# Kernel optimization log

Hardware: AMD Instinct MI355X
Metric: run time of the kernel (lower is better)

## Reference

```python
import jax, jax.numpy as jnp
import numpy as np

N = 50000
IN_CH = 128
HID = 32
HEADS = 3
OUT_CH = 128
E = 800000
NEG_SLOPE = 0.2
BN_EPS = 1e-5


def _glorot(key, shape):
    fan = shape[0] + shape[-1]
    s = jnp.sqrt(6.0 / fan)
    return jax.random.uniform(key, shape, jnp.float32, -s, s)


def setup_inputs() -> dict:
    key = jax.random.key(0)
    ks = jax.random.split(key, 12)
    x = jax.random.normal(ks[0], (N, IN_CH), jnp.float32)
    edge_index = jax.random.randint(ks[1], (2, E), 0, N, jnp.int64)
    # GATConv 1: in -> HID per head, HEADS heads, concat
    W1 = _glorot(ks[2], (IN_CH, HEADS * HID))
    att_src1 = _glorot(ks[3], (HEADS, HID))
    att_dst1 = _glorot(ks[4], (HEADS, HID))
    b1 = jnp.zeros((HEADS * HID,), jnp.float32)
    # GATConv 2: HEADS*HID -> OUT_CH, 1 head
    W2 = _glorot(ks[5], (HEADS * HID, OUT_CH))
    att_src2 = _glorot(ks[6], (1, OUT_CH))
    att_dst2 = _glorot(ks[7], (1, OUT_CH))
    b2 = jnp.zeros((OUT_CH,), jnp.float32)
    # BatchNorm params
    bn_gamma = jnp.ones((OUT_CH,), jnp.float32)
    bn_beta = jnp.zeros((OUT_CH,), jnp.float32)
    # residual Linear
    Wres = _glorot(ks[8], (IN_CH, OUT_CH))
    bres = jnp.zeros((OUT_CH,), jnp.float32)
    return dict(x=x, edge_index=edge_index, W1=W1, att_src1=att_src1,
                att_dst1=att_dst1, b1=b1, W2=W2, att_src2=att_src2,
                att_dst2=att_dst2, b2=b2, bn_gamma=bn_gamma, bn_beta=bn_beta,
                Wres=Wres, bres=bres)


def gat_conv(x, W, a_src, a_dst, b, src, dst, n, heads, ch):
    """PyG GATConv (eval mode, self-loops already in src/dst)."""
    h = (x @ W).reshape(n, heads, ch)                    # [N,H,C]
    a_s = jnp.sum(h * a_src[None], axis=-1)              # [N,H]
    a_d = jnp.sum(h * a_dst[None], axis=-1)              # [N,H]
    e = a_s[src] + a_d[dst]                              # [E,H]
    e = jnp.where(e > 0, e, NEG_SLOPE * e)               # leaky_relu
    m = jax.ops.segment_max(e, dst, num_segments=n)      # softmax over edges into dst
    e = jnp.exp(e - m[dst])
    denom = jax.ops.segment_sum(e, dst, num_segments=n)
    alpha = e / (denom[dst] + 1e-16)                     # [E,H]
    out = jax.ops.segment_sum(h[src] * alpha[:, :, None], dst, num_segments=n)
    return out.reshape(n, heads * ch) + b


def reference(x, edge_index, W1, att_src1, att_dst1, b1, W2, att_src2,
              att_dst2, b2, bn_gamma, bn_beta, Wres, bres):
    n = x.shape[0]
    loop = jnp.arange(n, dtype=edge_index.dtype)
    src = jnp.concatenate([edge_index[0], loop])         # add self-loops (PyG default)
    dst = jnp.concatenate([edge_index[1], loop])
    residual = x @ Wres + bres
    out = gat_conv(x, W1, att_src1, att_dst1, b1, src, dst, n, HEADS, HID)
    out = gat_conv(out, W2, att_src2, att_dst2, b2, src, dst, n, 1, OUT_CH)
    # BatchNorm1d, training-mode batch statistics
    mu = jnp.mean(out, axis=0)
    var = jnp.var(out, axis=0)
    out = (out - mu) * jax.lax.rsqrt(var + BN_EPS) * bn_gamma + bn_beta
    out = jax.nn.relu(out)
    return out + residual
```

## Files before the change

kernel.cpp:

```cpp
#include <hip/hip_runtime.h>

#define NEG 0.2f
#define NEG_INF (-1e30f)

typedef __attribute__((ext_vector_type(8))) short bf16x8;
typedef __attribute__((ext_vector_type(4))) float f32x4;

__device__ __forceinline__ float leaky(float e) { return e > 0.f ? e : NEG * e; }

__device__ __forceinline__ unsigned short f2bf(float f) {
    unsigned int u = __float_as_uint(f);
    unsigned int r = u + 0x7fffu + ((u >> 16) & 1u);
    return (unsigned short)(r >> 16);
}
__device__ __forceinline__ float2 bf2f2(unsigned int u) {
    float2 r;
    r.x = __uint_as_float(u << 16);
    r.y = __uint_as_float(u & 0xffff0000u);
    return r;
}

__device__ __forceinline__ void pack_w(const float* __restrict__ W,
                                       unsigned short* __restrict__ Bp, int K, int N, int idx) {
    int i = idx & 7;
    int rest = idx >> 3;
    int lane = rest & 63;
    rest >>= 6;
    int KT = K / 32;
    int kt = rest % KT;
    int ct = rest / KT;
    int m = lane & 15, kb = lane >> 4;
    int k = kt * 32 + kb * 8 + i, col = ct * 16 + m;
    Bp[idx] = f2bf(W[(size_t)k * N + col]);
}

__global__ __launch_bounds__(256) void prep_kernel(const float* __restrict__ x,
                                                   unsigned short* __restrict__ xb, int n4,
                                                   const float* __restrict__ W1,
                                                   unsigned short* __restrict__ w1p,
                                                   const float* __restrict__ W2,
                                                   unsigned short* __restrict__ w2p,
                                                   const float* __restrict__ Wres,
                                                   unsigned short* __restrict__ wresp,
                                                   const int* __restrict__ dst, int E,
                                                   int* __restrict__ bucketCnt, int nbk,
                                                   int binBlks) {
    int b = blockIdx.x;
    if (b < binBlks) {
        __shared__ int hist[1600];
        for (int k = threadIdx.x; k < nbk; k += 256) hist[k] = 0;
        __syncthreads();
        int c0 = b * 4096;
        int cnt = min(4096, E - c0);
        for (int i = threadIdx.x; i < cnt; i += 256)
            atomicAdd(&hist[dst[c0 + i] >> 5], 1);
        __syncthreads();
        for (int k = threadIdx.x; k < nbk; k += 256) {
            int h = hist[k];
            if (h) atomicAdd(&bucketCnt[k], h);
        }
        return;
    }
    b -= binBlks;
    int nxb = (n4 + 255) / 256;
    if (b < nxb) {
        int i = b * 256 + threadIdx.x;
        if (i < n4) {
            float4 v = ((const float4*)x)[i];
            ushort4 o;
            o.x = f2bf(v.x); o.y = f2bf(v.y); o.z = f2bf(v.z); o.w = f2bf(v.w);
            ((ushort4*)xb)[i] = o;
        }
        return;
    }
    b -= nxb;
    if (b < 48) { pack_w(W1, w1p, 128, 96, b * 256 + threadIdx.x); return; }
    b -= 48;
    if (b < 48) { pack_w(W2, w2p, 96, 128, b * 256 + threadIdx.x); return; }
    b -= 48;
    if (b < 64) { pack_w(Wres, wresp, 128, 128, b * 256 + threadIdx.x); }
}

__global__ __launch_bounds__(1024) void scan_buckets(const int* __restrict__ bc,
                                                     int* __restrict__ pairBase,
                                                     int* __restrict__ bcur,
                                                     int* __restrict__ offs, int nbk, int n,
                                                     float* __restrict__ part) {
    __shared__ int buf[1024];
    __shared__ int carry;
    int tid = threadIdx.x;
    for (int i = tid; i < 64 * 256; i += 1024) part[i] = 0.f;
    if (tid == 0) carry = 0;
    __syncthreads();
    for (int base = 0; base < nbk; base += 1024) {
        int v = (base + tid < nbk) ? bc[base + tid] : 0;
        buf[tid] = v;
        __syncthreads();
        for (int s = 1; s < 1024; s <<= 1) {
            int t = (tid >= s) ? buf[tid - s] : 0;
            __syncthreads();
            buf[tid] += t;
            __syncthreads();
        }
        int incl = buf[tid];
        int tot = buf[1023];
        int c = carry;
        if (base + tid < nbk) {
            int ex = c + incl - v;
            pairBase[base + tid] = ex;
            bcur[base + tid] = ex;
        }
        __syncthreads();
        if (tid == 0) carry = c + tot;
        __syncthreads();
    }
    if (tid == 0) {
        pairBase[nbk] = carry;
        offs[n] = carry;
    }
}

__global__ __launch_bounds__(256) void bin_kernel(const int* __restrict__ src,
                                                  const int* __restrict__ dst, int E,
                                                  int* __restrict__ bcur,
                                                  int2* __restrict__ pairBuf, int nb) {
    __shared__ int2 stage[4096];
    __shared__ int hist[1600];
    __shared__ int base[1600];
    for (int c0 = blockIdx.x * 4096; c0 < E; c0 += gridDim.x * 4096) {
        int cnt = min(4096, E - c0);
        for (int b = threadIdx.x; b < nb; b += 256) hist[b] = 0;
        __syncthreads();
        for (int i = threadIdx.x; i < cnt; i += 256) {
            int s = src[c0 + i], d = dst[c0 + i];
            stage[i] = make_int2(s, d);
            atomicAdd(&hist[d >> 5], 1);
        }
        __syncthreads();
        for (int b = threadIdx.x; b < nb; b += 256) {
            int h = hist[b];
            if (h) base[b] = atomicAdd(&bcur[b], h);
            hist[b] = 0;
        }
        __syncthreads();
        for (int i = threadIdx.x; i < cnt; i += 256) {
            int2 p = stage[i];
            int b = p.y >> 5;
            int off = atomicAdd(&hist[b], 1);
            pairBuf[base[b] + off] = p;
        }
        __syncthreads();
    }
}

template <int K, int N, int HEADS>
__device__ __forceinline__ void gemm_body(int w, const unsigned short* __restrict__ A,
                                          const unsigned short* __restrict__ Bp,
                                          const float* __restrict__ bias,
                                          unsigned short* __restrict__ outB,
                                          const float* __restrict__ asrc,
                                          const float* __restrict__ adst,
                                          float* __restrict__ a_s,
                                          float* __restrict__ a_d, int M) {
    constexpr int KT = K / 32, CT = N / 16;
    int row0 = w * 16;
    if (row0 >= M) return;
    int lane = threadIdx.x & 63;
    int m = lane & 15, kb = lane >> 4;
    const unsigned short* arow = A + (size_t)(row0 + m) * K + kb * 8;

    f32x4 acc[CT];
#pragma unroll
    for (int ct = 0; ct < CT; ++ct) acc[ct] = (f32x4){0.f, 0.f, 0.f, 0.f};

#pragma unroll
    for (int kt = 0; kt < KT; ++kt) {
        bf16x8 a = *(const bf16x8*)(arow + kt * 32);
#pragma unroll
        for (int ct = 0; ct < CT; ++ct) {
            bf16x8 b = *(const bf16x8*)(Bp + ((size_t)(ct * KT + kt) * 64 + lane) * 8);
            acc[ct] = __builtin_amdgcn_mfma_f32_16x16x32_bf16(a, b, acc[ct], 0, 0, 0);
        }
    }

#pragma unroll
    for (int r = 0; r < 4; ++r) {
        int row = row0 + kb * 4 + r;
#pragma unroll
        for (int ct = 0; ct < CT; ++ct) {
            int col = ct * 16 + m;
            float v = acc[ct][r] + (bias ? bias[col] : 0.f);
            outB[(size_t)row * N + col] = f2bf(v);
        }
    }

    if (HEADS > 0) {
        float asv[CT], adv[CT];
#pragma unroll
        for (int ct = 0; ct < CT; ++ct) {
            int col = ct * 16 + m;
            asv[ct] = asrc[col];
            adv[ct] = adst[col];
        }
        constexpr int TPH = CT / (HEADS > 0 ? HEADS : 1);
#pragma unroll
        for (int r = 0; r < 4; ++r) {
            int row = row0 + kb * 4 + r;
#pragma unroll
            for (int h = 0; h < HEADS; ++h) {
                float s = 0.f, d = 0.f;
#pragma unroll
                for (int t = 0; t < TPH; ++t) {
                    int ct = h * TPH + t;
                    s += acc[ct][r] * asv[ct];
                    d += acc[ct][r] * adv[ct];
                }
#pragma unroll
                for (int off = 1; off <= 8; off <<= 1) {
                    s += __shfl_xor(s, off);
                    d += __shfl_xor(d, off);
                }
                if (m == 0) {
                    a_s[(size_t)row * HEADS + h] = s;
                    a_d[(size_t)row * HEADS + h] = d;
                }
            }
        }
    }
}

__global__ __launch_bounds__(256) void phase2_kernel(
    const int2* __restrict__ pairBuf, const int* __restrict__ pairBase,
    const int* __restrict__ bcur, int* __restrict__ offs,
    int* __restrict__ csr, int nb,
    const unsigned short* __restrict__ xb,
    const unsigned short* __restrict__ w1p, unsigned short* __restrict__ h1b,
    const float* __restrict__ asrc1, const float* __restrict__ adst1,
    float* __restrict__ as1, float* __restrict__ ad1,
    const unsigned short* __restrict__ wresp, const float* __restrict__ bres,
    unsigned short* __restrict__ residb, int n, int passBlks, int g1Blks) {
    int b = blockIdx.x;
    int lane = threadIdx.x & 63;
    int wid = threadIdx.x >> 6;
    if (b < passBlks) {
        __shared__ int cnt[4][32];
        int bk = b * 4 + wid;
        if (bk < nb) {
            int node0 = bk * 32;
            int lo = pairBase[bk], hi = bcur[bk];
            if (lane < 32) cnt[wid][lane] = 0;
            for (int i = lo + lane; i < hi; i += 64)
                atomicAdd(&cnt[wid][pairBuf[i].y & 31], 1);
            int myc = (lane < 32) ? cnt[wid][lane] : 0;
            int c = myc;
#pragma unroll
            for (int s = 1; s < 32; s <<= 1) {
                int t = __shfl_up(c, s);
                if (lane >= s && lane < 32) c += t;
            }
            int basePos = lo + c - myc;
            if (lane < 32) {
                if (node0 + lane < n) offs[node0 + lane] = basePos;
                cnt[wid][lane] = basePos;
            }
            for (int i = lo + lane; i < hi; i += 64) {
                int2 p = pairBuf[i];
                int pos = atomicAdd(&cnt[wid][p.y & 31], 1);
                csr[pos] = p.x;
            }
        }
        return;
    }
    b -= passBlks;
    if (b < g1Blks) {
        gemm_body<128, 96, 3>(b * 4 + wid, xb, w1p, nullptr, h1b,
                              asrc1, adst1, as1, ad1, n);
        return;
    }
    b -= g1Blks;
    gemm_body<128, 128, 0>(b * 4 + wid, xb, wresp, bres, residb,
                           nullptr, nullptr, nullptr, nullptr, n);
}

__global__ __launch_bounds__(256) void gemm2_kernel(const unsigned short* __restrict__ A,
                                                    const unsigned short* __restrict__ Bp,
                                                    unsigned short* __restrict__ outB,
                                                    const float* __restrict__ asrc,
                                                    const float* __restrict__ adst,
                                                    float* __restrict__ a_s,
                                                    float* __restrict__ a_d, int M) {
    gemm_body<96, 128, 1>(blockIdx.x * 4 + (threadIdx.x >> 6), A, Bp, nullptr, outB,
                          asrc, adst, a_s, a_d, M);
}

__global__ __launch_bounds__(256) void gat1_agg(const unsigned short* __restrict__ h1b,
                                                const float* __restrict__ a_s,
                                                const float* __restrict__ a_d,
                                                const int* __restrict__ offs,
                                                const int* __restrict__ csr,
                                                const float* __restrict__ b1,
                                                unsigned short* __restrict__ out1b, int n) {
    __shared__ int ssrc[4][64];
    __shared__ float se[4][3][64];
    int wid = threadIdx.x >> 6;
    int node = blockIdx.x * 4 + wid;
    if (node >= n) return;
    int lane = threadIdx.x & 63;
    int head = lane >> 4; if (head > 2) head = 2;
    int beg = offs[node], end = offs[node + 1];
    int deg = end - beg;
    float ad0 = a_d[node * 3 + 0], ad1 = a_d[node * 3 + 1], ad2 = a_d[node * 3 + 2];
    float es0 = leaky(a_s[node * 3 + 0] + ad0);
    float es1 = leaky(a_s[node * 3 + 1] + ad1);
    float es2 = leaky(a_s[node * 3 + 2] + ad2);
    float2 hv0 = make_float2(0.f, 0.f);
    if (lane < 48) hv0 = bf2f2(*(const unsigned int*)&h1b[(size_t)node * 96 + 2 * lane]);

    float den;
    float2 acc;

    if (deg <= 64) {
        int s = 0;
        float l0 = NEG_INF, l1 = NEG_INF, l2 = NEG_INF;
        if (lane < deg) {
            s = csr[beg + lane];
            l0 = leaky(a_s[s * 3 + 0] + ad0);
            l1 = leaky(a_s[s * 3 + 1] + ad1);
            l2 = leaky(a_s[s * 3 + 2] + ad2);
        }
        float m0 = l0, m1 = l1, m2 = l2;
#pragma unroll
        for (int sh = 32; sh >= 1; sh >>= 1) {
            m0 = fmaxf(m0, __shfl_xor(m0, sh));
            m1 = fmaxf(m1, __shfl_xor(m1, sh));
            m2 = fmaxf(m2, __shfl_xor(m2, sh));
        }
        m0 = fmaxf(m0, es0); m1 = fmaxf(m1, es1); m2 = fmaxf(m2, es2);
        float e0 = 0.f, e1 = 0.f, e2 = 0.f;
        if (lane < deg) {
            e0 = __expf(l0 - m0); e1 = __expf(l1 - m1); e2 = __expf(l2 - m2);
        }
        ssrc[wid][lane] = s;
        se[wid][0][lane] = e0; se[wid][1][lane] = e1; se[wid][2][lane] = e2;
        float w0 = __expf(es0 - m0), w1 = __expf(es1 - m1), w2 = __expf(es2 - m2);
        den = (head == 0) ? w0 : ((head == 1) ? w1 : w2);
        float wSelf = (lane < 16) ? w0 : ((lane < 32) ? w1 : w2);
        acc.x = wSelf * hv0.x; acc.y = wSelf * hv0.y;

        int jj = 0;
        for (; jj + 7 < deg; jj += 8) {
            int sA[8]; float wA[8]; unsigned ph[8];
#pragma unroll
            for (int q = 0; q < 8; ++q) {
                sA[q] = ssrc[wid][jj + q];
                wA[q] = se[wid][head][jj + q];
            }
#pragma unroll
            for (int q = 0; q < 8; ++q)
                ph[q] = (lane < 48) ? *(const unsigned*)&h1b[(size_t)sA[q] * 96 + 2 * lane] : 0u;
            float dsum = 0.f;
#pragma unroll
            for (int q = 0; q < 8; ++q) {
                dsum += wA[q];
                if (lane < 48) {
                    float2 h = bf2f2(ph[q]);
                    acc.x += wA[q] * h.x; acc.y += wA[q] * h.y;
                }
            }
            den += dsum;
        }
        for (; jj + 3 < deg; jj += 4) {
            int sA[4]; float wA[4]; unsigned ph[4];
#pragma unroll
            for (int q = 0; q < 4; ++q) {
                sA[q] = ssrc[wid][jj + q];
                wA[q] = se[wid][head][jj + q];
            }
#pragma unroll
            for (int q = 0; q < 4; ++q)
                ph[q] = (lane < 48) ? *(const unsigned*)&h1b[(size_t)sA[q] * 96 + 2 * lane] : 0u;
            float dsum = 0.f;
#pragma unroll
            for (int q = 0; q < 4; ++q) {
                dsum += wA[q];
                if (lane < 48) {
                    float2 h = bf2f2(ph[q]);
                    acc.x += wA[q] * h.x; acc.y += wA[q] * h.y;
                }
            }
            den += dsum;
        }
        for (; jj < deg; ++jj) {
            int sA = ssrc[wid][jj];
            float wA = se[wid][head][jj];
            den += wA;
            if (lane < 48) {
                float2 ha = bf2f2(*(const unsigned*)&h1b[(size_t)sA * 96 + 2 * lane]);
                acc.x += wA * ha.x; acc.y += wA * ha.y;
            }
        }
    } else {
        float m0 = es0, m1 = es1, m2 = es2;
        for (int j = beg + lane; j < end; j += 64) {
            int s = csr[j];
            m0 = fmaxf(m0, leaky(a_s[s * 3 + 0] + ad0));
            m1 = fmaxf(m1, leaky(a_s[s * 3 + 1] + ad1));
            m2 = fmaxf(m2, leaky(a_s[s * 3 + 2] + ad2));
        }
#pragma unroll
        for (int sh = 32; sh >= 1; sh >>= 1) {
            m0 = fmaxf(m0, __shfl_xor(m0, sh));
            m1 = fmaxf(m1, __shfl_xor(m1, sh));
            m2 = fmaxf(m2, __shfl_xor(m2, sh));
        }
        float w0 = __expf(es0 - m0), w1 = __expf(es1 - m1), w2 = __expf(es2 - m2);
        den = (head == 0) ? w0 : ((head == 1) ? w1 : w2);
        float wSelf = (lane < 16) ? w0 : ((lane < 32) ? w1 : w2);
        acc.x = wSelf * hv0.x; acc.y = wSelf * hv0.y;
        for (int t0 = beg; t0 < end; t0 += 64) {
            int cnt = min(64, end - t0);
            int s = 0;
            float e0 = 0.f, e1 = 0.f, e2 = 0.f;
            if (lane < cnt) {
                s = csr[t0 + lane];
                e0 = __expf(leaky(a_s[s * 3 + 0] + ad0) - m0);
                e1 = __expf(leaky(a_s[s * 3 + 1] + ad1) - m1);
                e2 = __expf(leaky(a_s[s * 3 + 2] + ad2) - m2);
            }
            ssrc[wid][lane] = s;
            se[wid][0][lane] = e0; se[wid][1][lane] = e1; se[wid][2][lane] = e2;
            int jj = 0;
            for (; jj + 7 < cnt; jj += 8) {
                int sA[8]; float wA[8]; unsigned ph[8];
#pragma unroll
                for (int q = 0; q < 8; ++q) {
                    sA[q] = ssrc[wid][jj + q];
                    wA[q] = se[wid][head][jj + q];
                }
#pragma unroll
                for (int q = 0; q < 8; ++q)
                    ph[q] = (lane < 48) ? *(const unsigned*)&h1b[(size_t)sA[q] * 96 + 2 * lane] : 0u;
                float dsum = 0.f;
#pragma unroll
                for (int q = 0; q < 8; ++q) {
                    dsum += wA[q];
                    if (lane < 48) {
                        float2 h = bf2f2(ph[q]);
                        acc.x += wA[q] * h.x; acc.y += wA[q] * h.y;
                    }
                }
                den += dsum;
            }
            for (; jj < cnt; ++jj) {
                int sA = ssrc[wid][jj];
                float wA = se[wid][head][jj];
                den += wA;
                if (lane < 48) {
                    float2 ha = bf2f2(*(const unsigned*)&h1b[(size_t)sA * 96 + 2 * lane]);
                    acc.x += wA * ha.x; acc.y += wA * ha.y;
                }
            }
        }
    }

    if (lane < 48) {
        float inv = 1.f / (den + 1e-16f);
        ushort2 o;
        o.x = f2bf(acc.x * inv + b1[2 * lane]);
        o.y = f2bf(acc.y * inv + b1[2 * lane + 1]);
        *(ushort2*)&out1b[(size_t)node * 96 + 2 * lane] = o;
    }
}

__global__ __launch_bounds__(256) void gat2_agg(const unsigned short* __restrict__ h2b,
                                                const float* __restrict__ a_s,
                                                const float* __restrict__ a_d,
                                                const int* __restrict__ offs,
                                                const int* __restrict__ csr,
                                                const float* __restrict__ b2,
                                                unsigned short* __restrict__ out2b,
                                                float* __restrict__ part, int n) {
    __shared__ int ssrc[4][64];
    __shared__ float se[4][64];
    __shared__ float4 red[4][64];
    int wid = threadIdx.x >> 6;
    int node = blockIdx.x * 4 + wid;
    int lane = threadIdx.x & 63;
    float2 o = make_float2(0.f, 0.f);

    if (node < n) {
        int beg = offs[node], end = offs[node + 1];
        int deg = end - beg;
        float ad = a_d[node];
        float es = leaky(a_s[node] + ad);
        float2 hv0 = bf2f2(*(const unsigned int*)&h2b[(size_t)node * 128 + 2 * lane]);
        float den;
        float2 acc;

        if (deg <= 64) {
            int s = 0;
            float l = NEG_INF;
            if (lane < deg) {
                s = csr[beg + lane];
                l = leaky(a_s[s] + ad);
            }
            float m = l;
#pragma unroll
            for (int sh = 32; sh >= 1; sh >>= 1) m = fmaxf(m, __shfl_xor(m, sh));
            m = fmaxf(m, es);
            float e = (lane < deg) ? __expf(l - m) : 0.f;
            ssrc[wid][lane] = s;
            se[wid][lane] = e;
            float wSelf = __expf(es - m);
            den = wSelf;
            acc.x = wSelf * hv0.x; acc.y = wSelf * hv0.y;

            int jj = 0;
            for (; jj + 7 < deg; jj += 8) {
                int sA[8]; float wA[8]; unsigned ph[8];
#pragma unroll
                for (int q = 0; q < 8; ++q) {
                    sA[q] = ssrc[wid][jj + q];
                    wA[q] = se[wid][jj + q];
                }
#pragma unroll
                for (int q = 0; q < 8; ++q)
                    ph[q] = *(const unsigned*)&h2b[(size_t)sA[q] * 128 + 2 * lane];
                float dsum = 0.f;
#pragma unroll
                for (int q = 0; q < 8; ++q) {
                    dsum += wA[q];
                    float2 h = bf2f2(ph[q]);
                    acc.x += wA[q] * h.x; acc.y += wA[q] * h.y;
                }
                den += dsum;
            }
            for (; jj + 3 < deg; jj += 4) {
                int sA[4]; float wA[4]; unsigned ph[4];
#pragma unroll
                for (int q = 0; q < 4; ++q) {
                    sA[q] = ssrc[wid][jj + q];
                    wA[q] = se[wid][jj + q];
                }
#pragma unroll
                for (int q = 0; q < 4; ++q)
                    ph[q] = *(const unsigned*)&h2b[(size_t)sA[q] * 128 + 2 * lane];
                float dsum = 0.f;
#pragma unroll
                for (int q = 0; q < 4; ++q) {
                    dsum += wA[q];
                    float2 h = bf2f2(ph[q]);
                    acc.x += wA[q] * h.x; acc.y += wA[q] * h.y;
                }
                den += dsum;
            }
            for (; jj < deg; ++jj) {
                int sA = ssrc[wid][jj];
                float wA = se[wid][jj];
                den += wA;
                float2 ha = bf2f2(*(const unsigned*)&h2b[(size_t)sA * 128 + 2 * lane]);
                acc.x += wA * ha.x; acc.y += wA * ha.y;
            }
        } else {
            float m = es;
            for (int j = beg + lane; j < end; j += 64) {
                int s = csr[j];
                m = fmaxf(m, leaky(a_s[s] + ad));
            }
#pragma unroll
            for (int sh = 32; sh >= 1; sh >>= 1) m = fmaxf(m, __shfl_xor(m, sh));
            float wSelf = __expf(es - m);
            den = wSelf;
            acc.x = wSelf * hv0.x; acc.y = wSelf * hv0.y;
            for (int t0 = beg; t0 < end; t0 += 64) {
                int cnt = min(64, end - t0);
                int s = 0;
                float e = 0.f;
                if (lane < cnt) {
                    s = csr[t0 + lane];
                    e = __expf(leaky(a_s[s] + ad) - m);
                }
                ssrc[wid][lane] = s;
                se[wid][lane] = e;
                int jj = 0;
                for (; jj + 7 < cnt; jj += 8) {
                    int sA[8]; float wA[8]; unsigned ph[8];
#pragma unroll
                    for (int q = 0; q < 8; ++q) {
                        sA[q] = ssrc[wid][jj + q];
                        wA[q] = se[wid][jj + q];
                    }
#pragma unroll
                    for (int q = 0; q < 8; ++q)
                        ph[q] = *(const unsigned*)&h2b[(size_t)sA[q] * 128 + 2 * lane];
                    float dsum = 0.f;
#pragma unroll
                    for (int q = 0; q < 8; ++q) {
                        dsum += wA[q];
                        float2 h = bf2f2(ph[q]);
                        acc.x += wA[q] * h.x; acc.y += wA[q] * h.y;
                    }
                    den += dsum;
                }
                for (; jj < cnt; ++jj) {
                    int sA = ssrc[wid][jj];
                    float wA = se[wid][jj];
                    den += wA;
                    float2 ha = bf2f2(*(const unsigned*)&h2b[(size_t)sA * 128 + 2 * lane]);
                    acc.x += wA * ha.x; acc.y += wA * ha.y;
                }
            }
        }

        float inv = 1.f / (den + 1e-16f);
        o.x = acc.x * inv + b2[2 * lane];
        o.y = acc.y * inv + b2[2 * lane + 1];
        ushort2 ob;
        ob.x = f2bf(o.x); ob.y = f2bf(o.y);
        *(ushort2*)&out2b[(size_t)node * 128 + 2 * lane] = ob;
    }

    red[wid][lane] = make_float4(o.x, o.y, o.x * o.x, o.y * o.y);
    __syncthreads();
    if (wid == 0) {
        float4 a = red[0][lane], b = red[1][lane], c = red[2][lane], d = red[3][lane];
        float sx = a.x + b.x + c.x + d.x;
        float sy = a.y + b.y + c.y + d.y;
        float qx = a.z + b.z + c.z + d.z;
        float qy = a.w + b.w + c.w + d.w;
        float* p = part + (size_t)(blockIdx.x & 63) * 256;
        atomicAdd(&p[2 * lane + 0], sx);
        atomicAdd(&p[2 * lane + 1], sy);
        atomicAdd(&p[128 + 2 * lane + 0], qx);
        atomicAdd(&p[128 + 2 * lane + 1], qy);
    }
}

__global__ void bn_finalize(const float* __restrict__ part, const float* __restrict__ gamma,
                            const float* __restrict__ beta, float* __restrict__ ss, int n) {
    int c = threadIdx.x;
    float S = 0.f, Q = 0.f;
    for (int k = 0; k < 64; ++k) {
        S += part[(size_t)k * 256 + c];
        Q += part[(size_t)k * 256 + 128 + c];
    }
    float invN = 1.f / (float)n;
    float mu = S * invN;
    float var = Q * invN - mu * mu;
    float g = gamma[c] * rsqrtf(var + 1e-5f);
    ss[c] = g;
    ss[128 + c] = beta[c] - mu * g;
}

__global__ void final_kernel(const unsigned short* __restrict__ out2b,
                             const unsigned short* __restrict__ residb,
                             const float* __restrict__ ss, float* __restrict__ out, int n) {
    int i = blockIdx.x * blockDim.x + threadIdx.x;
    if (i >= n * 32) return;
    int c0 = (i & 31) * 4;
    uint2 v = ((const uint2*)out2b)[i];
    uint2 r = ((const uint2*)residb)[i];
    float2 v01 = bf2f2(v.x), v23 = bf2f2(v.y);
    float2 r01 = bf2f2(r.x), r23 = bf2f2(r.y);
    float4 o;
    o.x = fmaxf(v01.x * ss[c0 + 0] + ss[128 + c0 + 0], 0.f) + r01.x;
    o.y = fmaxf(v01.y * ss[c0 + 1] + ss[128 + c0 + 1], 0.f) + r01.y;
    o.z = fmaxf(v23.x * ss[c0 + 2] + ss[128 + c0 + 2], 0.f) + r23.x;
    o.w = fmaxf(v23.y * ss[c0 + 3] + ss[128 + c0 + 3], 0.f) + r23.y;
    ((float4*)out)[i] = o;
}

extern "C" void kernel_launch(void* const* d_in, const int* in_sizes, int n_in,
                              void* d_out, int out_size, void* d_ws, size_t ws_size,
                              hipStream_t stream) {
    const float* x     = (const float*)d_in[0];
    const int*   ei    = (const int*)d_in[1];
    const float* W1    = (const float*)d_in[2];
    const float* asrc1 = (const float*)d_in[3];
    const float* adst1 = (const float*)d_in[4];
    const float* b1    = (const float*)d_in[5];
    const float* W2    = (const float*)d_in[6];
    const float* asrc2 = (const float*)d_in[7];
    const float* adst2 = (const float*)d_in[8];
    const float* b2    = (const float*)d_in[9];
    const float* gamma = (const float*)d_in[10];
    const float* beta  = (const float*)d_in[11];
    const float* Wres  = (const float*)d_in[12];
    const float* bres  = (const float*)d_in[13];

    const int n = in_sizes[0] / 128;
    const int E = in_sizes[1] / 2;

    char* ws = (char*)d_ws;
    size_t off = 0;
    auto alloc = [&](size_t bytes) {
        void* p = ws + off;
        off = (off + bytes + 255) & ~(size_t)255;
        return p;
    };
    float* as1  = (float*)alloc((size_t)n * 3 * 4);
    float* ad1  = (float*)alloc((size_t)n * 3 * 4);
    float* as2  = (float*)alloc((size_t)n * 4);
    float* ad2  = (float*)alloc((size_t)n * 4);
    float* part = (float*)alloc(64 * 256 * 4);
    float* ss   = (float*)alloc(256 * 4);
    unsigned short* xb     = (unsigned short*)alloc((size_t)n * 128 * 2);
    unsigned short* h1b    = (unsigned short*)alloc((size_t)n * 96 * 2);
    unsigned short* h2b    = (unsigned short*)alloc((size_t)n * 128 * 2);
    unsigned short* out1b  = (unsigned short*)alloc((size_t)n * 96 * 2);
    unsigned short* out2b  = (unsigned short*)alloc((size_t)n * 128 * 2);
    unsigned short* residb = (unsigned short*)alloc((size_t)n * 128 * 2);
    unsigned short* w1p    = (unsigned short*)alloc(128 * 96 * 2);
    unsigned short* w2p    = (unsigned short*)alloc(96 * 128 * 2);
    unsigned short* wresp  = (unsigned short*)alloc(128 * 128 * 2);
    int* offs      = (int*)alloc((size_t)(n + 1) * 4);
    int* bucketCnt = (int*)alloc(1600 * 4);
    int* pairBase  = (int*)alloc(1601 * 4);
    int* bcur      = (int*)alloc(1600 * 4);
    int2* pairBuf  = (int2*)alloc((size_t)E * 8);
    int* csr       = (int*)alloc((size_t)E * 4);

    hipMemsetAsync(bucketCnt, 0, 1600 * 4, stream);

    const int* srcIdx = ei;
    const int* dstIdx = ei + E;
    const int NB = (n + 31) / 32;
    const int binBlks = (E + 4095) / 4096;

    const int nxb = (n * 32 + 255) / 256;
    prep_kernel<<<binBlks + nxb + 160, 256, 0, stream>>>(x, xb, n * 32, W1, w1p, W2, w2p,
                                                         Wres, wresp, dstIdx, E,
                                                         bucketCnt, NB, binBlks);

    scan_buckets<<<1, 1024, 0, stream>>>(bucketCnt, pairBase, bcur, offs, NB, n, part);

    bin_kernel<<<binBlks, 256, 0, stream>>>(srcIdx, dstIdx, E, bcur, pairBuf, NB);

    const int mt = (n + 15) / 16;
    const int gblk = (mt + 3) / 4;
    const int passBlks = 391;

    phase2_kernel<<<passBlks + 2 * gblk, 256, 0, stream>>>(
        pairBuf, pairBase, bcur, offs, csr, NB, xb, w1p, h1b, asrc1, adst1, as1, ad1,
        wresp, bres, residb, n, passBlks, gblk);

    gat1_agg<<<(n + 3) / 4, 256, 0, stream>>>(h1b, as1, ad1, offs, csr, b1, out1b, n);
    gemm2_kernel<<<gblk, 256, 0, stream>>>(out1b, w2p, h2b, asrc2, adst2, as2, ad2, n);
    gat2_agg<<<(n + 3) / 4, 256, 0, stream>>>(h2b, as2, ad2, offs, csr, b2, out2b, part, n);
    bn_finalize<<<1, 128, 0, stream>>>(part, gamma, beta, ss, n);
    final_kernel<<<(n * 32 + 255) / 256, 256, 0, stream>>>(out2b, residb, ss, (float*)d_out, n);
}
```

Measured before the change: 163.9 us.

## Split wavefront into two halves processing alternate edges with 8-byte gathers

Both GAT aggregation kernels now split each 64-lane wave into two halves that process alternate neighbor edges, with each lane gathering 4 bf16 features (8 bytes) instead of 2. The two halves' partial sums are combined with a cross-half shuffle at the end. The softmax denominator is now computed with a wave reduction over the exp values instead of being accumulated serially in the gather loop. This is meant to double the number of edge gathers in flight and widen the loads, in exchange for extra shuffles and reworked BN partial-sum bookkeeping.

```diff
diff --git a/kernel.cpp b/kernel.cpp
--- a/kernel.cpp
+++ b/kernel.cpp
@@ -306,18 +306,21 @@
     int node = blockIdx.x * 4 + wid;
     if (node >= n) return;
     int lane = threadIdx.x & 63;
-    int head = lane >> 4; if (head > 2) head = 2;
+    int half = lane >> 5;
+    int cl = lane & 31;
+    int c4 = cl * 4;
+    bool act = cl < 24;
+    int head4 = act ? (cl >> 3) : 2;
+
     int beg = offs[node], end = offs[node + 1];
     int deg = end - beg;
     float ad0 = a_d[node * 3 + 0], ad1 = a_d[node * 3 + 1], ad2 = a_d[node * 3 + 2];
     float es0 = leaky(a_s[node * 3 + 0] + ad0);
     float es1 = leaky(a_s[node * 3 + 1] + ad1);
     float es2 = leaky(a_s[node * 3 + 2] + ad2);
-    float2 hv0 = make_float2(0.f, 0.f);
-    if (lane < 48) hv0 = bf2f2(*(const unsigned int*)&h1b[(size_t)node * 96 + 2 * lane]);
-
-    float den;
-    float2 acc;
+
+    float den0, den1, den2;
+    float a0 = 0.f, a1 = 0.f, a2 = 0.f, a3 = 0.f;
 
     if (deg <= 64) {
         int s = 0;
@@ -342,61 +345,53 @@
         }
         ssrc[wid][lane] = s;
         se[wid][0][lane] = e0; se[wid][1][lane] = e1; se[wid][2][lane] = e2;
+        float d0 = e0, d1 = e1, d2 = e2;
+#pragma unroll
+        for (int sh = 32; sh >= 1; sh >>= 1) {
+            d0 += __shfl_xor(d0, sh);
+            d1 += __shfl_xor(d1, sh);
+            d2 += __shfl_xor(d2, sh);
+        }
         float w0 = __expf(es0 - m0), w1 = __expf(es1 - m1), w2 = __expf(es2 - m2);
-        den = (head == 0) ? w0 : ((head == 1) ? w1 : w2);
-        float wSelf = (lane < 16) ? w0 : ((lane < 32) ? w1 : w2);
-        acc.x = wSelf * hv0.x; acc.y = wSelf * hv0.y;
-
+        den0 = d0 + w0; den1 = d1 + w1; den2 = d2 + w2;
+        if (half == 0 && act) {
+            uint2 hv = *(const uint2*)&h1b[(size_t)node * 96 + c4];
+            float wS = (head4 == 0) ? w0 : ((head4 == 1) ? w1 : w2);
+            float2 x01 = bf2f2(hv.x), x23 = bf2f2(hv.y);
+            a0 = wS * x01.x; a1 = wS * x01.y; a2 = wS * x23.x; a3 = wS * x23.y;
+        }
         int jj = 0;
         for (; jj + 7 < deg; jj += 8) {
-            int sA[8]; float wA[8]; unsigned ph[8];
-#pragma unroll
-            for (int q = 0; q < 8; ++q) {
-                sA[q] = ssrc[wid][jj + q];
-                wA[q] = se[wid][head][jj + q];
-            }
-#pragma unroll
-            for (int q = 0; q < 8; ++q)
-                ph[q] = (lane < 48) ? *(const unsigned*)&h1b[(size_t)sA[q] * 96 + 2 * lane] : 0u;
-            float dsum = 0.f;
-#pragma unroll
-            for (int q = 0; q < 8; ++q) {
-                dsum += wA[q];
-                if (lane < 48) {
-                    float2 h = bf2f2(ph[q]);
-                    acc.x += wA[q] * h.x; acc.y += wA[q] * h.y;
-                }
-            }
-            den += dsum;
-        }
-        for (; jj + 3 < deg; jj += 4) {
-            int sA[4]; float wA[4]; unsigned ph[4];
-#pragma unroll
-            for (int q = 0; q < 4; ++q) {
-                sA[q] = ssrc[wid][jj + q];
-                wA[q] = se[wid][head][jj + q];
-            }
-#pragma unroll
-            for (int q = 0; q < 4; ++q)
-                ph[q] = (lane < 48) ? *(const unsigned*)&h1b[(size_t)sA[q] * 96 + 2 * lane] : 0u;
-            float dsum = 0.f;
-#pragma unroll
-            for (int q = 0; q < 4; ++q) {
-                dsum += wA[q];
-                if (lane < 48) {
-                    float2 h = bf2f2(ph[q]);
-                    acc.x += wA[q] * h.x; acc.y += wA[q] * h.y;
-                }
-            }
-            den += dsum;
-        }
-        for (; jj < deg; ++jj) {
-            int sA = ssrc[wid][jj];
-            float wA = se[wid][head][jj];
-            den += wA;
-            if (lane < 48) {
-                float2 ha = bf2f2(*(const unsigned*)&h1b[(size_t)sA * 96 + 2 * lane]);
-                acc.x += wA * ha.x; acc.y += wA * ha.y;
+            int eA = jj + half, eB = jj + 2 + half, eC = jj + 4 + half, eD = jj + 6 + half;
+            int sA = ssrc[wid][eA], sB = ssrc[wid][eB];
+            int sC = ssrc[wid][eC], sD = ssrc[wid][eD];
+            float wA = se[wid][head4][eA], wB = se[wid][head4][eB];
+            float wC = se[wid][head4][eC], wD = se[wid][head4][eD];
+            uint2 pA = make_uint2(0, 0), pB = pA, pC = pA, pD = pA;
+            if (act) {
+                pA = *(const uint2*)&h1b[(size_t)sA * 96 + c4];
+                pB = *(const uint2*)&h1b[(size_t)sB * 96 + c4];
+                pC = *(const uint2*)&h1b[(size_t)sC * 96 + c4];
+                pD = *(const uint2*)&h1b[(size_t)sD * 96 + c4];
+            }
+            float2 x01, x23;
+            x01 = bf2f2(pA.x); x23 = bf2f2(pA.y);
+            a0 += wA * x01.x; a1 += wA * x01.y; a2 += wA * x23.x; a3 += wA * x23.y;
+            x01 = bf2f2(pB.x); x23 = bf2f2(pB.y);
+            a0 += wB * x01.x; a1 += wB * x01.y; a2 += wB * x23.x; a3 += wB * x23.y;
+            x01 = bf2f2(pC.x); x23 = bf2f2(pC.y);
+            a0 += wC * x01.x; a1 += wC * x01.y; a2 += wC * x23.x; a3 += wC * x23.y;
+            x01 = bf2f2(pD.x); x23 = bf2f2(pD.y);
+            a0 += wD * x01.x; a1 += wD * x01.y; a2 += wD * x23.x; a3 += wD * x23.y;
+        }
+        for (; jj < deg; jj += 2) {
+            int eA = jj + half;
+            int sA = ssrc[wid][eA];
+            float wA = se[wid][head4][eA];
+            if (act) {
+                uint2 p = *(const uint2*)&h1b[(size_t)sA * 96 + c4];
+                float2 x01 = bf2f2(p.x), x23 = bf2f2(p.y);
+                a0 += wA * x01.x; a1 += wA * x01.y; a2 += wA * x23.x; a3 += wA * x23.y;
             }
         }
     } else {
@@ -414,9 +409,13 @@
             m2 = fmaxf(m2, __shfl_xor(m2, sh));
         }
         float w0 = __expf(es0 - m0), w1 = __expf(es1 - m1), w2 = __expf(es2 - m2);
-        den = (head == 0) ? w0 : ((head == 1) ? w1 : w2);
-        float wSelf = (lane < 16) ? w0 : ((lane < 32) ? w1 : w2);
-        acc.x = wSelf * hv0.x; acc.y = wSelf * hv0.y;
+        den0 = w0; den1 = w1; den2 = w2;
+        if (half == 0 && act) {
+            uint2 hv = *(const uint2*)&h1b[(size_t)node * 96 + c4];
+            float wS = (head4 == 0) ? w0 : ((head4 == 1) ? w1 : w2);
+            float2 x01 = bf2f2(hv.x), x23 = bf2f2(hv.y);
+            a0 = wS * x01.x; a1 = wS * x01.y; a2 = wS * x23.x; a3 = wS * x23.y;
+        }
         for (int t0 = beg; t0 < end; t0 += 64) {
             int cnt = min(64, end - t0);
             int s = 0;
@@ -429,46 +428,64 @@
             }
             ssrc[wid][lane] = s;
             se[wid][0][lane] = e0; se[wid][1][lane] = e1; se[wid][2][lane] = e2;
+            float d0 = e0, d1 = e1, d2 = e2;
+#pragma unroll
+            for (int sh = 32; sh >= 1; sh >>= 1) {
+                d0 += __shfl_xor(d0, sh);
+                d1 += __shfl_xor(d1, sh);
+                d2 += __shfl_xor(d2, sh);
+            }
+            den0 += d0; den1 += d1; den2 += d2;
             int jj = 0;
             for (; jj + 7 < cnt; jj += 8) {
-                int sA[8]; float wA[8]; unsigned ph[8];
-#pragma unroll
-                for (int q = 0; q < 8; ++q) {
-                    sA[q] = ssrc[wid][jj + q];
-                    wA[q] = se[wid][head][jj + q];
+                int eA = jj + half, eB = jj + 2 + half, eC = jj + 4 + half, eD = jj + 6 + half;
+                int sA = ssrc[wid][eA], sB = ssrc[wid][eB];
+                int sC = ssrc[wid][eC], sD = ssrc[wid][eD];
+                float wA = se[wid][head4][eA], wB = se[wid][head4][eB];
+                float wC = se[wid][head4][eC], wD = se[wid][head4][eD];
+                uint2 pA = make_uint2(0, 0), pB = pA, pC = pA, pD = pA;
+                if (act) {
+                    pA = *(const uint2*)&h1b[(size_t)sA * 96 + c4];
+                    pB = *(const uint2*)&h1b[(size_t)sB * 96 + c4];
+                    pC = *(const uint2*)&h1b[(size_t)sC * 96 + c4];
+                    pD = *(const uint2*)&h1b[(size_t)sD * 96 + c4];
                 }
-#pragma unroll
-                for (int q = 0; q < 8; ++q)
-                    ph[q] = (lane < 48) ? *(const unsigned*)&h1b[(size_t)sA[q] * 96 + 2 * lane] : 0u;
-                float dsum = 0.f;
-#pragma unroll
-                for (int q = 0; q < 8; ++q) {
-                    dsum += wA[q];
-                    if (lane < 48) {
-                        float2 h = bf2f2(ph[q]);
-                        acc.x += wA[q] * h.x; acc.y += wA[q] * h.y;
-                    }
+                float2 x01, x23;
+                x01 = bf2f2(pA.x); x23 = bf2f2(pA.y);
+                a0 += wA * x01.x; a1 += wA * x01.y; a2 += wA * x23.x; a3 += wA * x23.y;
+                x01 = bf2f2(pB.x); x23 = bf2f2(pB.y);
+                a0 += wB * x01.x; a1 += wB * x01.y; a2 += wB * x23.x; a3 += wB * x23.y;
+                x01 = bf2f2(pC.x); x23 = bf2f2(pC.y);
+                a0 += wC * x01.x; a1 += wC * x01.y; a2 += wC * x23.x; a3 += wC * x23.y;
+                x01 = bf2f2(pD.x); x23 = bf2f2(pD.y);
+                a0 += wD * x01.x; a1 += wD * x01.y; a2 += wD * x23.x; a3 += wD * x23.y;
+            }
+            for (; jj < cnt; jj += 2) {
+                int eA = jj + half;
+                int sA = ssrc[wid][eA];
+                float wA = se[wid][head4][eA];
+                if (act) {
+                    uint2 p = *(const uint2*)&h1b[(size_t)sA * 96 + c4];
+                    float2 x01 = bf2f2(p.x), x23 = bf2f2(p.y);
+                    a0 += wA * x01.x; a1 += wA * x01.y; a2 += wA * x23.x; a3 += wA * x23.y;
                 }
-                den += dsum;
-            }
-            for (; jj < cnt; ++jj) {
-                int sA = ssrc[wid][jj];
-                float wA = se[wid][head][jj];
-                den += wA;
-                if (lane < 48) {
-                    float2 ha = bf2f2(*(const unsigned*)&h1b[(size_t)sA * 96 + 2 * lane]);
-                    acc.x += wA * ha.x; acc.y += wA * ha.y;
-                }
-            }
-        }
-    }
-
-    if (lane < 48) {
+            }
+        }
+    }
+
+    a0 += __shfl_xor(a0, 32);
+    a1 += __shfl_xor(a1, 32);
+    a2 += __shfl_xor(a2, 32);
+    a3 += __shfl_xor(a3, 32);
+    if (half == 0 && act) {
+        float den = (head4 == 0) ? den0 : ((head4 == 1) ? den1 : den2);
         float inv = 1.f / (den + 1e-16f);
-        ushort2 o;
-        o.x = f2bf(acc.x * inv + b1[2 * lane]);
-        o.y = f2bf(acc.y * inv + b1[2 * lane + 1]);
-        *(ushort2*)&out1b[(size_t)node * 96 + 2 * lane] = o;
+        ushort4 o;
+        o.x = f2bf(a0 * inv + b1[c4 + 0]);
+        o.y = f2bf(a1 * inv + b1[c4 + 1]);
+        o.z = f2bf(a2 * inv + b1[c4 + 2]);
+        o.w = f2bf(a3 * inv + b1[c4 + 3]);
+        *(ushort4*)&out1b[(size_t)node * 96 + c4] = o;
     }
 }
 
@@ -482,20 +499,24 @@
                                                 float* __restrict__ part, int n) {
     __shared__ int ssrc[4][64];
     __shared__ float se[4][64];
-    __shared__ float4 red[4][64];
+    __shared__ float4 reds[4][32];
+    __shared__ float4 redq[4][32];
     int wid = threadIdx.x >> 6;
     int node = blockIdx.x * 4 + wid;
     int lane = threadIdx.x & 63;
-    float2 o = make_float2(0.f, 0.f);
-
-    if (node < n) {
+    int half = lane >> 5;
+    int cl = lane & 31;
+    int c4 = cl * 4;
+    bool valid = node < n;
+
+    float den = 0.f;
+    float a0 = 0.f, a1 = 0.f, a2 = 0.f, a3 = 0.f;
+
+    if (valid) {
         int beg = offs[node], end = offs[node + 1];
         int deg = end - beg;
         float ad = a_d[node];
         float es = leaky(a_s[node] + ad);
-        float2 hv0 = bf2f2(*(const unsigned int*)&h2b[(size_t)node * 128 + 2 * lane]);
-        float den;
-        float2 acc;
 
         if (deg <= 64) {
             int s = 0;
@@ -511,55 +532,44 @@
             float e = (lane < deg) ? __expf(l - m) : 0.f;
             ssrc[wid][lane] = s;
             se[wid][lane] = e;
+            float d = e;
+#pragma unroll
+            for (int sh = 32; sh >= 1; sh >>= 1) d += __shfl_xor(d, sh);
             float wSelf = __expf(es - m);
-            den = wSelf;
-            acc.x = wSelf * hv0.x; acc.y = wSelf * hv0.y;
-
+            den = d + wSelf;
+            if (half == 0) {
+                uint2 hv = *(const uint2*)&h2b[(size_t)node * 128 + c4];
+                float2 x01 = bf2f2(hv.x), x23 = bf2f2(hv.y);
+                a0 = wSelf * x01.x; a1 = wSelf * x01.y; a2 = wSelf * x23.x; a3 = wSelf * x23.y;
+            }
             int jj = 0;
             for (; jj + 7 < deg; jj += 8) {
-                int sA[8]; float wA[8]; unsigned ph[8];
-#pragma unroll
-                for (int q = 0; q < 8; ++q) {
-                    sA[q] = ssrc[wid][jj + q];
-                    wA[q] = se[wid][jj + q];
-                }
-#pragma unroll
-                for (int q = 0; q < 8; ++q)
-                    ph[q] = *(const unsigned*)&h2b[(size_t)sA[q] * 128 + 2 * lane];
-                float dsum = 0.f;
-#pragma unroll
-                for (int q = 0; q < 8; ++q) {
-                    dsum += wA[q];
-                    float2 h = bf2f2(ph[q]);
-                    acc.x += wA[q] * h.x; acc.y += wA[q] * h.y;
-                }
-                den += dsum;
-            }
-            for (; jj + 3 < deg; jj += 4) {
-                int sA[4]; float wA[4]; unsigned ph[4];
-#pragma unroll
-                for (int q = 0; q < 4; ++q) {
-                    sA[q] = ssrc[wid][jj + q];
-                    wA[q] = se[wid][jj + q];
-                }
-#pragma unroll
-                for (int q = 0; q < 4; ++q)
-                    ph[q] = *(const unsigned*)&h2b[(size_t)sA[q] * 128 + 2 * lane];
-                float dsum = 0.f;
-#pragma unroll
-                for (int q = 0; q < 4; ++q) {
-                    dsum += wA[q];
-                    float2 h = bf2f2(ph[q]);
-                    acc.x += wA[q] * h.x; acc.y += wA[q] * h.y;
-                }
-                den += dsum;
-            }
-            for (; jj < deg; ++jj) {
-                int sA = ssrc[wid][jj];
-                float wA = se[wid][jj];
-                den += wA;
-                float2 ha = bf2f2(*(const unsigned*)&h2b[(size_t)sA * 128 + 2 * lane]);
-                acc.x += wA * ha.x; acc.y += wA * ha.y;
+                int eA = jj + half, eB = jj + 2 + half, eC = jj + 4 + half, eD = jj + 6 + half;
+                int sA = ssrc[wid][eA], sB = ssrc[wid][eB];
+                int sC = ssrc[wid][eC], sD = ssrc[wid][eD];
+                float wA = se[wid][eA], wB = se[wid][eB];
+                float wC = se[wid][eC], wD = se[wid][eD];
+                uint2 pA = *(const uint2*)&h2b[(size_t)sA * 128 + c4];
+                uint2 pB = *(const uint2*)&h2b[(size_t)sB * 128 + c4];
+                uint2 pC = *(const uint2*)&h2b[(size_t)sC * 128 + c4];
+                uint2 pD = *(const uint2*)&h2b[(size_t)sD * 128 + c4];
+                float2 x01, x23;
+                x01 = bf2f2(pA.x); x23 = bf2f2(pA.y);
+                a0 += wA * x01.x; a1 += wA * x01.y; a2 += wA * x23.x; a3 += wA * x23.y;
+                x01 = bf2f2(pB.x); x23 = bf2f2(pB.y);
+                a0 += wB * x01.x; a1 += wB * x01.y; a2 += wB * x23.x; a3 += wB * x23.y;
+                x01 = bf2f2(pC.x); x23 = bf2f2(pC.y);
+                a0 += wC * x01.x; a1 += wC * x01.y; a2 += wC * x23.x; a3 += wC * x23.y;
+                x01 = bf2f2(pD.x); x23 = bf2f2(pD.y);
+                a0 += wD * x01.x; a1 += wD * x01.y; a2 += wD * x23.x; a3 += wD * x23.y;
+            }
+            for (; jj < deg; jj += 2) {
+                int eA = jj + half;
+                int sA = ssrc[wid][eA];
+                float wA = se[wid][eA];
+                uint2 p = *(const uint2*)&h2b[(size_t)sA * 128 + c4];
+                float2 x01 = bf2f2(p.x), x23 = bf2f2(p.y);
+                a0 += wA * x01.x; a1 += wA * x01.y; a2 += wA * x23.x; a3 += wA * x23.y;
             }
         } else {
             float m = es;
@@ -571,7 +581,11 @@
             for (int sh = 32; sh >= 1; sh >>= 1) m = fmaxf(m, __shfl_xor(m, sh));
             float wSelf = __expf(es - m);
             den = wSelf;
-            acc.x = wSelf * hv0.x; acc.y = wSelf * hv0.y;
+            if (half == 0) {
+                uint2 hv = *(const uint2*)&h2b[(size_t)node * 128 + c4];
+                float2 x01 = bf2f2(hv.x), x23 = bf2f2(hv.y);
+                a0 = wSelf * x01.x; a1 = wSelf * x01.y; a2 = wSelf * x23.x; a3 = wSelf * x23.y;
+            }
             for (int t0 = beg; t0 < end; t0 += 64) {
                 int cnt = min(64, end - t0);
                 int s = 0;
@@ -582,57 +596,82 @@
                 }
                 ssrc[wid][lane] = s;
                 se[wid][lane] = e;
+                float d = e;
+#pragma unroll
+                for (int sh = 32; sh >= 1; sh >>= 1) d += __shfl_xor(d, sh);
+                den += d;
                 int jj = 0;
                 for (; jj + 7 < cnt; jj += 8) {
-                    int sA[8]; float wA[8]; unsigned ph[8];
-#pragma unroll
-                    for (int q = 0; q < 8; ++q) {
-                        sA[q] = ssrc[wid][jj + q];
-                        wA[q] = se[wid][jj + q];
-                    }
-#pragma unroll
-                    for (int q = 0; q < 8; ++q)
-                        ph[q] = *(const unsigned*)&h2b[(size_t)sA[q] * 128 + 2 * lane];
-                    float dsum = 0.f;
-#pragma unroll
-                    for (int q = 0; q < 8; ++q) {
-                        dsum += wA[q];
-                        float2 h = bf2f2(ph[q]);
-                        acc.x += wA[q] * h.x; acc.y += wA[q] * h.y;
-                    }
-                    den += dsum;
+                    int eA = jj + half, eB = jj + 2 + half, eC = jj + 4 + half, eD = jj + 6 + half;
+                    int sA = ssrc[wid][eA], sB = ssrc[wid][eB];
+                    int sC = ssrc[wid][eC], sD = ssrc[wid][eD];
+                    float wA = se[wid][eA], wB = se[wid][eB];
+                    float wC = se[wid][eC], wD = se[wid][eD];
+                    uint2 pA = *(const uint2*)&h2b[(size_t)sA * 128 + c4];
+                    uint2 pB = *(const uint2*)&h2b[(size_t)sB * 128 + c4];
+                    uint2 pC = *(const uint2*)&h2b[(size_t)sC * 128 + c4];
+                    uint2 pD = *(const uint2*)&h2b[(size_t)sD * 128 + c4];
+                    float2 x01, x23;
+                    x01 = bf2f2(pA.x); x23 = bf2f2(pA.y);
+                    a0 += wA * x01.x; a1 += wA * x01.y; a2 += wA * x23.x; a3 += wA * x23.y;
+                    x01 = bf2f2(pB.x); x23 = bf2f2(pB.y);
+                    a0 += wB * x01.x; a1 += wB * x01.y; a2 += wB * x23.x; a3 += wB * x23.y;
+                    x01 = bf2f2(pC.x); x23 = bf2f2(pC.y);
+                    a0 += wC * x01.x; a1 += wC * x01.y; a2 += wC * x23.x; a3 += wC * x23.y;
+                    x01 = bf2f2(pD.x); x23 = bf2f2(pD.y);
+                    a0 += wD * x01.x; a1 += wD * x01.y; a2 += wD * x23.x; a3 += wD * x23.y;
                 }
-                for (; jj < cnt; ++jj) {
-                    int sA = ssrc[wid][jj];
-                    float wA = se[wid][jj];
-                    den += wA;
-                    float2 ha = bf2f2(*(const unsigned*)&h2b[(size_t)sA * 128 + 2 * lane]);
-                    acc.x += wA * ha.x; acc.y += wA * ha.y;
+                for (; jj < cnt; jj += 2) {
+                    int eA = jj + half;
+                    int sA = ssrc[wid][eA];
+                    float wA = se[wid][eA];
+                    uint2 p = *(const uint2*)&h2b[(size_t)sA * 128 + c4];
+                    float2 x01 = bf2f2(p.x), x23 = bf2f2(p.y);
+                    a0 += wA * x01.x; a1 += wA * x01.y; a2 += wA * x23.x; a3 += wA * x23.y;
                 }
             }
         }
-
-        float inv = 1.f / (den + 1e-16f);
-        o.x = acc.x * inv + b2[2 * lane];
-        o.y = acc.y * inv + b2[2 * lane + 1];
-        ushort2 ob;
-        ob.x = f2bf(o.x); ob.y = f2bf(o.y);
-        *(ushort2*)&out2b[(size_t)node * 128 + 2 * lane] = ob;
-    }
-
-    red[wid][lane] = make_float4(o.x, o.y, o.x * o.x, o.y * o.y);
+    }
+
+    a0 += __shfl_xor(a0, 32);
+    a1 += __shfl_xor(a1, 32);
+    a2 += __shfl_xor(a2, 32);
+    a3 += __shfl_xor(a3, 32);
+
+    float o0 = 0.f, o1 = 0.f, o2 = 0.f, o3 = 0.f;
+    if (half == 0) {
+        if (valid) {
+            float inv = 1.f / (den + 1e-16f);
+            o0 = a0 * inv + b2[c4 + 0];
+            o1 = a1 * inv + b2[c4 + 1];
+            o2 = a2 * inv + b2[c4 + 2];
+            o3 = a3 * inv + b2[c4 + 3];
+            ushort4 ob;
+            ob.x = f2bf(o0); ob.y = f2bf(o1); ob.z = f2bf(o2); ob.w = f2bf(o3);
+            *(ushort4*)&out2b[(size_t)node * 128 + c4] = ob;
+        }
+        reds[wid][cl] = make_float4(o0, o1, o2, o3);
+        redq[wid][cl] = make_float4(o0 * o0, o1 * o1, o2 * o2, o3 * o3);
+    }
     __syncthreads();
-    if (wid == 0) {
-        float4 a = red[0][lane], b = red[1][lane], c = red[2][lane], d = red[3][lane];
-        float sx = a.x + b.x + c.x + d.x;
-        float sy = a.y + b.y + c.y + d.y;
-        float qx = a.z + b.z + c.z + d.z;
-        float qy = a.w + b.w + c.w + d.w;
+    if (wid == 0 && lane < 32) {
+        float4 S = reds[0][lane], Q = redq[0][lane];
+#pragma unroll
+        for (int k = 1; k < 4; ++k) {
+            float4 s2 = reds[k][lane], q2 = redq[k][lane];
+            S.x += s2.x; S.y += s2.y; S.z += s2.z; S.w += s2.w;
+            Q.x += q2.x; Q.y += q2.y; Q.z += q2.z; Q.w += q2.w;
+        }
         float* p = part + (size_t)(blockIdx.x & 63) * 256;
-        atomicAdd(&p[2 * lane + 0], sx);
-        atomicAdd(&p[2 * lane + 1], sy);
-        atomicAdd(&p[128 + 2 * lane + 0], qx);
-        atomicAdd(&p[128 + 2 * lane + 1], qy);
+        int c = lane * 4;
+        atomicAdd(&p[c + 0], S.x);
+        atomicAdd(&p[c + 1], S.y);
+        atomicAdd(&p[c + 2], S.z);
+        atomicAdd(&p[c + 3], S.w);
+        atomicAdd(&p[128 + c + 0], Q.x);
+        atomicAdd(&p[128 + c + 1], Q.y);
+        atomicAdd(&p[128 + c + 2], Q.z);
+        atomicAdd(&p[128 + c + 3], Q.w);
     }
 }
 
```

Result: slower. 183.1 us (+11.7%).
